# Kernel tuning notes

Hardware: AMD Instinct MI355X
Metric: run time of the kernel (lower is better)

The kernel has to match this reference:

```python
import jax, jax.numpy as jnp
import numpy as np

D_MODEL = 1024
N_HEADS = 16
HEAD_DIM = D_MODEL // N_HEADS


def setup_inputs() -> dict:
    key = jax.random.key(0)
    ks = jax.random.split(key, 10)
    s = 1.0 / np.sqrt(D_MODEL)
    inp = {
        "ts_features": jax.random.normal(ks[0], (8, 512, D_MODEL), dtype=jnp.float32),
        "llm_features": jax.random.normal(ks[1], (8, 2048, D_MODEL), dtype=jnp.float32),
        "q_w": jax.random.uniform(ks[2], (D_MODEL, D_MODEL), jnp.float32, -s, s),
        "q_b": jax.random.uniform(ks[3], (D_MODEL,), jnp.float32, -s, s),
        "k_w": jax.random.uniform(ks[4], (D_MODEL, D_MODEL), jnp.float32, -s, s),
        "k_b": jax.random.uniform(ks[5], (D_MODEL,), jnp.float32, -s, s),
        "v_w": jax.random.uniform(ks[6], (D_MODEL, D_MODEL), jnp.float32, -s, s),
        "v_b": jax.random.uniform(ks[7], (D_MODEL,), jnp.float32, -s, s),
        "o_w": jax.random.uniform(ks[8], (D_MODEL, D_MODEL), jnp.float32, -s, s),
        "o_b": jax.random.uniform(ks[9], (D_MODEL,), jnp.float32, -s, s),
    }
    return inp


def reference(ts_features, llm_features, q_w, q_b, k_w, k_b, v_w, v_b, o_w, o_b):
    B, P, _ = ts_features.shape
    S = llm_features.shape[1]
    # Linear projections (torch Linear: x @ W^T + b); split heads -> [B, H, L, Dh]
    q = (ts_features @ q_w.T + q_b).reshape(B, P, N_HEADS, HEAD_DIM).transpose(0, 2, 1, 3)
    k = (llm_features @ k_w.T + k_b).reshape(B, S, N_HEADS, HEAD_DIM).transpose(0, 2, 1, 3)
    v = (llm_features @ v_w.T + v_b).reshape(B, S, N_HEADS, HEAD_DIM).transpose(0, 2, 1, 3)
    # Full attention: scores [B, H, P, S]
    scores = jnp.einsum("bhpd,bhsd->bhps", q, k) / np.sqrt(HEAD_DIM).astype(np.float32)
    attn = jax.nn.softmax(scores, axis=-1)  # dropout is identity in eval mode
    context = jnp.einsum("bhps,bhsd->bhpd", attn, v)
    context = context.transpose(0, 2, 1, 3).reshape(B, P, D_MODEL)
    return context @ o_w.T + o_b
```

## Files before the change

### kernel.cpp

```cpp
#include <hip/hip_runtime.h>

#define DM 1024
#define B_ 8
#define P_ 512
#define S_ 2048

typedef __bf16 bf16;
typedef __bf16 bf16x4 __attribute__((ext_vector_type(4)));
typedef __bf16 bf16x8 __attribute__((ext_vector_type(8)));
typedef float f32x4 __attribute__((ext_vector_type(4)));
typedef float f32x16 __attribute__((ext_vector_type(16)));

__device__ __forceinline__ void gload_lds16(const void* g, void* l) {
  __builtin_amdgcn_global_load_lds(
      (const __attribute__((address_space(1))) unsigned int*)g,
      (__attribute__((address_space(3))) unsigned int*)l, 16, 0, 0);
}

__device__ __forceinline__ f32x4 mfma16(bf16x8 a, bf16x8 b, f32x4 c) {
  return __builtin_amdgcn_mfma_f32_16x16x32_bf16(a, b, c, 0, 0, 0);
}
__device__ __forceinline__ f32x16 mfma32(bf16x8 a, bf16x8 b, f32x16 c) {
  return __builtin_amdgcn_mfma_f32_32x32x16_bf16(a, b, c, 0, 0, 0);
}

__device__ __forceinline__ unsigned cvt_pk_bf16(float lo, float hi) {
  unsigned r;
  asm("v_cvt_pk_bf16_f32 %0, %1, %2" : "=v"(r) : "v"(lo), "v"(hi));
  return r;
}
__device__ __forceinline__ void plswap(unsigned& a, unsigned& b) {
  asm volatile("s_nop 1\n\tv_permlane32_swap_b32 %0, %1" : "+v"(a), "+v"(b));
}
__device__ __forceinline__ void bar() {
  asm volatile("" ::: "memory");
  __builtin_amdgcn_s_barrier();
  asm volatile("" ::: "memory");
}

union U8 { unsigned u[4]; bf16x8 v; };

#define QSCALE 0.18033688011112042f

__global__ void cvt_all(const float* __restrict__ ts, const float* __restrict__ llm,
                        const float* __restrict__ qw, const float* __restrict__ kw,
                        const float* __restrict__ vw, const float* __restrict__ ow,
                        bf16* __restrict__ ts_o, bf16* __restrict__ llm_o,
                        bf16* __restrict__ qw_o, bf16* __restrict__ kw_o,
                        bf16* __restrict__ vw_o, bf16* __restrict__ ow_o) {
  const int total = 24 << 18;
  int i = blockIdx.x * blockDim.x + threadIdx.x;
  const int stride = gridDim.x * blockDim.x;
  for (; i < total; i += stride) {
    int r = i >> 18;
    const float* in;
    bf16* out;
    int off;
    if (r < 4) { in = ts; out = ts_o; off = i; }
    else if (r < 20) { in = llm; out = llm_o; off = i - (4 << 18); }
    else if (r == 20) { in = qw; out = qw_o; off = i - (20 << 18); }
    else if (r == 21) { in = kw; out = kw_o; off = i - (21 << 18); }
    else if (r == 22) { in = vw; out = vw_o; off = i - (22 << 18); }
    else { in = ow; out = ow_o; off = i - (23 << 18); }
    float4 v = reinterpret_cast<const float4*>(in)[off];
    bf16x4 o;
    o[0] = (bf16)v.x; o[1] = (bf16)v.y; o[2] = (bf16)v.z; o[3] = (bf16)v.w;
    reinterpret_cast<bf16x4*>(out)[off] = o;
  }
}

enum { MODE_F32 = 0, MODE_Q = 1 };

template <int MODE>
__global__ __launch_bounds__(256) void gemm_bt(
    const bf16* __restrict__ A, const bf16* __restrict__ Bw,
    const float* __restrict__ bias, void* __restrict__ out) {
  __shared__ char As[16384];
  __shared__ char Bs[16384];
  const int tid = threadIdx.x;
  const int w = tid >> 6, lane = tid & 63;
  const int g = lane >> 4, l15 = lane & 15;
  const int tn = blockIdx.x, tm = blockIdx.y;
  const int wm = w >> 1, wn = w & 1;

  f32x4 acc[4][4] = {};

  const char* Abase = (const char*)A + (size_t)(tm * 128) * (DM * 2);
  const char* Bbase = (const char*)Bw + (size_t)(tn * 128) * (DM * 2);

  for (int kt = 0; kt < DM / 64; ++kt) {
#pragma unroll
    for (int i = 0; i < 4; ++i) {
      int f = (w * 4 + i) * 1024 + lane * 16;
      int row = f >> 7;
      int kb = f & 127;
      int src = kb ^ ((row & 7) << 4);
      gload_lds16(Abase + (size_t)row * (DM * 2) + kt * 128 + src, As + (w * 4 + i) * 1024);
      gload_lds16(Bbase + (size_t)row * (DM * 2) + kt * 128 + src, Bs + (w * 4 + i) * 1024);
    }
    __syncthreads();
#pragma unroll
    for (int kk = 0; kk < 2; ++kk) {
      bf16x8 af[4], bfr[4];
#pragma unroll
      for (int mi = 0; mi < 4; ++mi) {
        int row = wm * 64 + mi * 16 + l15;
        int off = row * 128 + ((kk * 64 + g * 16) ^ ((row & 7) << 4));
        af[mi] = *reinterpret_cast<const bf16x8*>(As + off);
      }
#pragma unroll
      for (int ni = 0; ni < 4; ++ni) {
        int row = wn * 64 + ni * 16 + l15;
        int off = row * 128 + ((kk * 64 + g * 16) ^ ((row & 7) << 4));
        bfr[ni] = *reinterpret_cast<const bf16x8*>(Bs + off);
      }
#pragma unroll
      for (int mi = 0; mi < 4; ++mi)
#pragma unroll
        for (int ni = 0; ni < 4; ++ni)
          acc[mi][ni] = mfma16(af[mi], bfr[ni], acc[mi][ni]);
    }
    __syncthreads();
  }

#pragma unroll
  for (int mi = 0; mi < 4; ++mi) {
#pragma unroll
    for (int ni = 0; ni < 4; ++ni) {
      const int n = tn * 128 + wn * 64 + ni * 16 + l15;
      const float bn = bias[n];
      const int mb = tm * 128 + wm * 64 + mi * 16 + g * 4;
#pragma unroll
      for (int r = 0; r < 4; ++r) {
        const int m = mb + r;
        const float v = acc[mi][ni][r] + bn;
        if constexpr (MODE == MODE_F32) {
          ((float*)out)[(size_t)m * 1024 + n] = v;
        } else {
          const int b = m >> 9, p = m & 511, h = n >> 6, d = n & 63;
          ((bf16*)out)[((size_t)((b * 16 + h) * 512 + p)) * 64 + d] = (bf16)(v * QSCALE);
        }
      }
    }
  }
}

__global__ __launch_bounds__(512, 2) void gemm256kv(
    const bf16* __restrict__ A, const bf16* __restrict__ Bw,
    const float* __restrict__ kb, const float* __restrict__ vb,
    bf16* __restrict__ Kout, bf16* __restrict__ VTout) {
  __shared__ char lds[131072];
  const int tid = threadIdx.x;
  const int w = tid >> 6, lane = tid & 63;
  const int g = lane >> 4, l15 = lane & 15;
  const int wm = w >> 2, wn = w & 3;

  const int id = blockIdx.x;
  const int nid = (id & 7) * 64 + (id >> 3);
  const int tn = nid & 7, tm = nid >> 3;

  const int f0 = tid * 16, f1 = f0 + 8192;
  const int r0 = f0 >> 7, r1 = f1 >> 7;
  const size_t so0 = (size_t)r0 * 2048 + ((f0 & 127) ^ ((r0 & 7) << 4));
  const size_t so1 = (size_t)r1 * 2048 + ((f1 & 127) ^ ((r1 & 7) << 4));

  const char* Ab = (const char*)A + (size_t)(tm * 256) * 2048;
  const char* Bb = (const char*)Bw + (size_t)(tn * 256) * 2048;

#define STG(OP, HALF, KT)                                                      \
  {                                                                            \
    const char* base = ((OP) ? Bb : Ab) + (size_t)((HALF) * 128) * 2048 +      \
                       (size_t)(KT) * 128;                                     \
    char* dst = lds + (OP) * 65536 + ((((KT) & 1) * 2 + (HALF)) * 16384);      \
    gload_lds16(base + so0, dst + f0);                                         \
    gload_lds16(base + so1, dst + f1);                                         \
  }

  f32x4 acc[8][4] = {};
  bf16x8 a[4][2], b0[2][2], b1[2][2];

#define RD_A(MH)                                                               \
  _Pragma("unroll") for (int mi = 0; mi < 4; ++mi) _Pragma("unroll")           \
      for (int kk = 0; kk < 2; ++kk) {                                         \
    int lr = (MH) * 64 + mi * 16 + l15;                                        \
    int off = (((unsigned)(kt & 1) * 2 + wm) * 16384) + lr * 128 +             \
              ((kk * 64 + g * 16) ^ ((lr & 7) << 4));                          \
    a[mi][kk] = *reinterpret_cast<const bf16x8*>(lds + off);                   \
  }
#define RD_B(NH, DST)                                                          \
  _Pragma("unroll") for (int ni = 0; ni < 2; ++ni) _Pragma("unroll")           \
      for (int kk = 0; kk < 2; ++kk) {                                         \
    int lr = (wn & 1) * 64 + ((NH) * 2 + ni) * 16 + l15;                       \
    int off = 65536 + (((unsigned)(kt & 1) * 2 + (wn >> 1)) * 16384) +         \
              lr * 128 + ((kk * 64 + g * 16) ^ ((lr & 7) << 4));               \
    DST[ni][kk] = *reinterpret_cast<const bf16x8*>(lds + off);                 \
  }
#define MM(MH, NH, B)                                                          \
  __builtin_amdgcn_s_setprio(1);                                              \
  _Pragma("unroll") for (int mi = 0; mi < 4; ++mi) _Pragma("unroll")           \
      for (int ni = 0; ni < 2; ++ni) _Pragma("unroll")                         \
      for (int kk = 0; kk < 2; ++kk)                                           \
          acc[(MH)*4 + mi][(NH)*2 + ni] =                                      \
              mfma16(a[mi][kk], B[ni][kk], acc[(MH)*4 + mi][(NH)*2 + ni]);     \
  __builtin_amdgcn_s_setprio(0);

  STG(0, 0, 0); STG(1, 0, 0); STG(0, 1, 0); STG(1, 1, 0);
  STG(1, 1, 1); STG(0, 0, 1); STG(1, 0, 1);
  asm volatile("s_waitcnt vmcnt(6)" ::: "memory");
  bar();

  for (int kt = 0; kt < 16; ++kt) {
    RD_A(0); RD_B(0, b0);
    if (kt + 1 < 16) STG(0, 1, kt + 1);
    bar();
    MM(0, 0, b0);
    bar();
    RD_B(1, b1);
    bar();
    MM(0, 1, b1);
    bar();
    RD_A(1);
    if (kt + 2 < 16) STG(1, 1, kt + 2);
    bar();
    MM(1, 0, b0);
    bar();
    if (kt + 2 < 16) { STG(0, 0, kt + 2); STG(1, 0, kt + 2); }
    if (kt < 14) {
      asm volatile("s_waitcnt vmcnt(6)" ::: "memory");
    } else {
      asm volatile("s_waitcnt vmcnt(0)" ::: "memory");
    }
    bar();
    MM(1, 1, b1);
    bar();
  }

#pragma unroll
  for (int am = 0; am < 8; ++am) {
#pragma unroll
    for (int an = 0; an < 4; ++an) {
      const int n = tn * 256 + wn * 64 + an * 16 + l15;
      const int mb = tm * 256 + wm * 128 + am * 16 + g * 4;
      const int b = mb >> 11, s = mb & 2047;
      if (n >= 1024) {
        const int h = (n - 1024) >> 6, d = (n - 1024) & 63;
        const float bn = vb[n - 1024];
        bf16x4 pk;
#pragma unroll
        for (int r = 0; r < 4; ++r) pk[r] = (bf16)(acc[am][an][r] + bn);
        *reinterpret_cast<bf16x4*>(VTout + ((size_t)((b * 16 + h) * 64 + d)) * 2048 + s) = pk;
      } else {
        const int h = n >> 6, d = n & 63;
        const float bn = kb[n];
#pragma unroll
        for (int r = 0; r < 4; ++r)
          Kout[((size_t)((b * 16 + h) * 2048 + s + r)) * 64 + d] =
              (bf16)(acc[am][an][r] + bn);
      }
    }
  }
#undef STG
#undef RD_A
#undef RD_B
#undef MM
}

__global__ __launch_bounds__(256) void attn_kernel(
    const bf16* __restrict__ Q, const bf16* __restrict__ K,
    const bf16* __restrict__ VT, bf16* __restrict__ ctx) {
  __shared__ char lds[65536];
  const int tid = threadIdx.x;
  const int w = tid >> 6, lane = tid & 63;
  const int l31 = lane & 31, hi = lane >> 5;

  const int n = blockIdx.x;
  const int xcd = n & 7, mm = n >> 3;
  const int bh = xcd + ((mm >> 2) << 3);
  const int qt = mm & 3;
  const int q0 = qt * 128;

  const char* Kb = (const char*)(K + (size_t)bh * 2048 * 64);
  const char* Vb = (const char*)(VT + (size_t)bh * 64 * 2048);

  const char* Qrow = (const char*)(Q + ((size_t)bh * 512 + q0 + w * 32 + l31) * 64);
  bf16x8 qf[4];
#pragma unroll
  for (int kk = 0; kk < 4; ++kk)
    qf[kk] = *reinterpret_cast<const bf16x8*>(Qrow + kk * 32 + hi * 16);

  float lrun = 0.f;
  f32x16 oacc[2] = {};

#define STAGE(S0, BUF)                                                        \
  {                                                                           \
    _Pragma("unroll") for (int i = 0; i < 4; ++i) {                           \
      int f = i * 4096 + (w * 64 + lane) * 16;                                \
      int krow = f >> 7, kbyte = f & 127;                                     \
      gload_lds16(Kb + (size_t)((S0) + krow) * 128 +                          \
                      (kbyte ^ ((krow & 7) << 4)),                            \
                  (BUF) + i * 4096 + w * 1024);                               \
      int vrow = f >> 8, vbyte = f & 255;                                     \
      gload_lds16(Vb + (size_t)vrow * 4096 + (size_t)(S0) * 2 +               \
                      (vbyte ^ ((vrow & 7) << 4)),                            \
                  (BUF) + 16384 + i * 4096 + w * 1024);                       \
    }                                                                         \
  }

#define SUBTILE(T2, CUR)                                                      \
  {                                                                           \
    f32x16 sa[2] = {};                                                        \
    __builtin_amdgcn_s_setprio(1);                                            \
    _Pragma("unroll") for (int t = 0; t < 2; ++t) {                           \
      _Pragma("unroll") for (int kk = 0; kk < 4; ++kk) {                      \
        int row = (T2) * 64 + t * 32 + l31;                                   \
        int off = row * 128 + ((kk * 32 + hi * 16) ^ ((row & 7) << 4));       \
        bf16x8 kf = *reinterpret_cast<const bf16x8*>((CUR) + off);            \
        sa[t] = mfma32(kf, qf[kk], sa[t]);                                    \
      }                                                                       \
    }                                                                         \
    __builtin_amdgcn_s_setprio(0);                                            \
    bf16x8 vf[8];                                                             \
    _Pragma("unroll") for (int dt = 0; dt < 2; ++dt)                          \
        _Pragma("unroll") for (int ks = 0; ks < 4; ++ks) {                    \
      int row = dt * 32 + l31;                                                \
      int col = (T2) * 128 + ks * 32 + hi * 16;                               \
      int off = 16384 + row * 256 + (col ^ ((row & 7) << 4));                 \
      vf[dt * 4 + ks] = *reinterpret_cast<const bf16x8*>((CUR) + off);        \
    }                                                                         \
    bf16x8 pf[4];                                                             \
    _Pragma("unroll") for (int t = 0; t < 2; ++t)                             \
        _Pragma("unroll") for (int h2 = 0; h2 < 2; ++h2) {                    \
      float p[8];                                                             \
      _Pragma("unroll") for (int j = 0; j < 8; ++j) {                         \
        p[j] = __builtin_amdgcn_exp2f(sa[t][8 * h2 + j]);                     \
        lrun += p[j];                                                         \
      }                                                                       \
      unsigned a0 = cvt_pk_bf16(p[0], p[1]);                                  \
      unsigned a1 = cvt_pk_bf16(p[2], p[3]);                                  \
      unsigned a2 = cvt_pk_bf16(p[4], p[5]);                                  \
      unsigned a3 = cvt_pk_bf16(p[6], p[7]);                                  \
      plswap(a0, a2);                                                         \
      plswap(a1, a3);                                                         \
      U8 u;                                                                   \
      u.u[0] = a0; u.u[1] = a1; u.u[2] = a2; u.u[3] = a3;                     \
      pf[t * 2 + h2] = u.v;                                                   \
    }                                                                         \
    __builtin_amdgcn_s_setprio(1);                                            \
    _Pragma("unroll") for (int dt = 0; dt < 2; ++dt)                          \
        _Pragma("unroll") for (int ks = 0; ks < 4; ++ks)                      \
            oacc[dt] = mfma32(vf[dt * 4 + ks], pf[ks], oacc[dt]);             \
    __builtin_amdgcn_s_setprio(0);                                            \
  }

  STAGE(0, lds);

  for (int c = 0; c < 16; ++c) {
    char* cur = lds + (c & 1) * 32768;
    if (c + 1 < 16) {
      STAGE((c + 1) * 128, lds + ((c + 1) & 1) * 32768);
      asm volatile("s_waitcnt vmcnt(8)" ::: "memory");
    } else {
      asm volatile("s_waitcnt vmcnt(0)" ::: "memory");
    }
    bar();

    SUBTILE(0, cur);
    SUBTILE(1, cur);

    bar();
  }

  lrun += __shfl_xor(lrun, 32);
  const float inv = 1.0f / lrun;
  const int b = bh >> 4, h = bh & 15;
  const int prow = q0 + w * 32 + l31;
  bf16* dst = ctx + ((size_t)(b * 512 + prow)) * 1024 + h * 64;
#pragma unroll
  for (int dt = 0; dt < 2; ++dt)
#pragma unroll
    for (int g4 = 0; g4 < 4; ++g4) {
      bf16x4 pk4;
#pragma unroll
      for (int r = 0; r < 4; ++r) pk4[r] = (bf16)(oacc[dt][g4 * 4 + r] * inv);
      *reinterpret_cast<bf16x4*>(dst + dt * 32 + g4 * 8 + hi * 4) = pk4;
    }
#undef STAGE
#undef SUBTILE
}

extern "C" void kernel_launch(void* const* d_in, const int* in_sizes, int n_in,
                              void* d_out, int out_size, void* d_ws, size_t ws_size,
                              hipStream_t stream) {
  const float* ts = (const float*)d_in[0];
  const float* llm = (const float*)d_in[1];
  const float* qw = (const float*)d_in[2];
  const float* qb = (const float*)d_in[3];
  const float* kw = (const float*)d_in[4];
  const float* kb = (const float*)d_in[5];
  const float* vw = (const float*)d_in[6];
  const float* vb = (const float*)d_in[7];
  const float* ow = (const float*)d_in[8];
  const float* ob = (const float*)d_in[9];

  char* ws = (char*)d_ws;
  bf16* ts_bf = (bf16*)(ws + (0ull << 20));
  bf16* llm_bf = (bf16*)(ws + (8ull << 20));
  bf16* qw_bf = (bf16*)(ws + (40ull << 20));
  bf16* kw_bf = (bf16*)(ws + (42ull << 20));
  bf16* vw_bf = (bf16*)(ws + (44ull << 20));
  bf16* ow_bf = (bf16*)(ws + (46ull << 20));
  bf16* Qb = (bf16*)(ws + (48ull << 20));
  bf16* Kb = (bf16*)(ws + (56ull << 20));
  bf16* VTb = (bf16*)(ws + (88ull << 20));
  bf16* ctx = (bf16*)(ws + (120ull << 20));

  cvt_all<<<2048, 256, 0, stream>>>(ts, llm, qw, kw, vw, ow,
                                    ts_bf, llm_bf, qw_bf, kw_bf, vw_bf, ow_bf);

  gemm_bt<MODE_Q><<<dim3(8, 32), 256, 0, stream>>>(ts_bf, qw_bf, qb, Qb);
  gemm256kv<<<512, 512, 0, stream>>>(llm_bf, kw_bf, kb, vb, Kb, VTb);
  attn_kernel<<<512, 256, 0, stream>>>(Qb, Kb, VTb, ctx);
  gemm_bt<MODE_F32><<<dim3(8, 32), 256, 0, stream>>>(ctx, ow_bf, ob, (void*)d_out);
}
```

Measured before the change: 193.7 us.

## Split attention over key halves and double query rows per wave with combine pass

The attention kernel now has each wave process 64 query rows (two 32-row groups) that share each K/V fragment load. The key sequence is split into two halves across blocks, so the grid stays at 512 blocks. Each block writes unnormalized fp32 partial outputs and row sums, and a new combine kernel adds the halves, normalizes, and writes bf16 context. This halves LDS K/V traffic per query row, at the cost of an extra kernel launch, fp32 partial round-trip traffic, and higher register pressure with launch bounds of 2. The partial buffers reuse workspace from the ts/llm bf16 copies, which are already consumed by then.

```diff
diff --git a/kernel.cpp b/kernel.cpp
--- a/kernel.cpp
+++ b/kernel.cpp
@@ -265,31 +265,36 @@
 #undef MM
 }
 
-__global__ __launch_bounds__(256) void attn_kernel(
+__global__ __launch_bounds__(256, 2) void attn_kernel(
     const bf16* __restrict__ Q, const bf16* __restrict__ K,
-    const bf16* __restrict__ VT, bf16* __restrict__ ctx) {
+    const bf16* __restrict__ VT, float* __restrict__ Opart,
+    float* __restrict__ lpart) {
   __shared__ char lds[65536];
   const int tid = threadIdx.x;
   const int w = tid >> 6, lane = tid & 63;
   const int l31 = lane & 31, hi = lane >> 5;
 
   const int n = blockIdx.x;
-  const int xcd = n & 7, mm = n >> 3;
-  const int bh = xcd + ((mm >> 2) << 3);
-  const int qt = mm & 3;
-  const int q0 = qt * 128;
+  const int wid = (n & 7) * 64 + (n >> 3);
+  const int bh = wid >> 2;
+  const int qh = (wid >> 1) & 1;
+  const int sh = wid & 1;
+  const int q0 = qh * 256;
+  const int sbase = sh * 1024;
 
   const char* Kb = (const char*)(K + (size_t)bh * 2048 * 64);
   const char* Vb = (const char*)(VT + (size_t)bh * 64 * 2048);
 
-  const char* Qrow = (const char*)(Q + ((size_t)bh * 512 + q0 + w * 32 + l31) * 64);
-  bf16x8 qf[4];
-#pragma unroll
-  for (int kk = 0; kk < 4; ++kk)
-    qf[kk] = *reinterpret_cast<const bf16x8*>(Qrow + kk * 32 + hi * 16);
-
-  float lrun = 0.f;
-  f32x16 oacc[2] = {};
+  const char* QrowA = (const char*)(Q + ((size_t)bh * 512 + q0 + w * 64 + l31) * 64);
+  bf16x8 qfA[4], qfB[4];
+#pragma unroll
+  for (int kk = 0; kk < 4; ++kk) {
+    qfA[kk] = *reinterpret_cast<const bf16x8*>(QrowA + kk * 32 + hi * 16);
+    qfB[kk] = *reinterpret_cast<const bf16x8*>(QrowA + 4096 + kk * 32 + hi * 16);
+  }
+
+  float lrunA = 0.f, lrunB = 0.f;
+  f32x16 oaccA[2] = {}, oaccB[2] = {};
 
 #define STAGE(S0, BUF)                                                        \
   {                                                                           \
@@ -306,58 +311,69 @@
     }                                                                         \
   }
 
+#define SOFTMAX(SA, PF, LRUN)                                                 \
+  _Pragma("unroll") for (int t = 0; t < 2; ++t)                               \
+      _Pragma("unroll") for (int h2 = 0; h2 < 2; ++h2) {                      \
+    float p[8];                                                               \
+    _Pragma("unroll") for (int j = 0; j < 8; ++j) {                           \
+      p[j] = __builtin_amdgcn_exp2f(SA[t][8 * h2 + j]);                       \
+      LRUN += p[j];                                                           \
+    }                                                                         \
+    unsigned a0 = cvt_pk_bf16(p[0], p[1]);                                    \
+    unsigned a1 = cvt_pk_bf16(p[2], p[3]);                                    \
+    unsigned a2 = cvt_pk_bf16(p[4], p[5]);                                    \
+    unsigned a3 = cvt_pk_bf16(p[6], p[7]);                                    \
+    plswap(a0, a2);                                                           \
+    plswap(a1, a3);                                                           \
+    U8 u;                                                                     \
+    u.u[0] = a0; u.u[1] = a1; u.u[2] = a2; u.u[3] = a3;                       \
+    PF[t * 2 + h2] = u.v;                                                     \
+  }
+
 #define SUBTILE(T2, CUR)                                                      \
   {                                                                           \
+    bf16x8 kf[8];                                                             \
+    _Pragma("unroll") for (int t = 0; t < 2; ++t)                             \
+        _Pragma("unroll") for (int kk = 0; kk < 4; ++kk) {                    \
+      int row = (T2) * 64 + t * 32 + l31;                                     \
+      int off = row * 128 + ((kk * 32 + hi * 16) ^ ((row & 7) << 4));         \
+      kf[t * 4 + kk] = *reinterpret_cast<const bf16x8*>((CUR) + off);         \
+    }                                                                         \
     f32x16 sa[2] = {};                                                        \
     __builtin_amdgcn_s_setprio(1);                                            \
-    _Pragma("unroll") for (int t = 0; t < 2; ++t) {                           \
-      _Pragma("unroll") for (int kk = 0; kk < 4; ++kk) {                      \
-        int row = (T2) * 64 + t * 32 + l31;                                   \
-        int off = row * 128 + ((kk * 32 + hi * 16) ^ ((row & 7) << 4));       \
-        bf16x8 kf = *reinterpret_cast<const bf16x8*>((CUR) + off);            \
-        sa[t] = mfma32(kf, qf[kk], sa[t]);                                    \
-      }                                                                       \
-    }                                                                         \
+    _Pragma("unroll") for (int t = 0; t < 2; ++t)                             \
+        _Pragma("unroll") for (int kk = 0; kk < 4; ++kk)                      \
+            sa[t] = mfma32(kf[t * 4 + kk], qfA[kk], sa[t]);                   \
     __builtin_amdgcn_s_setprio(0);                                            \
-    bf16x8 vf[8];                                                             \
+    bf16x8 pfA[4];                                                            \
+    SOFTMAX(sa, pfA, lrunA);                                                  \
+    f32x16 sb[2] = {};                                                        \
+    __builtin_amdgcn_s_setprio(1);                                            \
+    _Pragma("unroll") for (int t = 0; t < 2; ++t)                             \
+        _Pragma("unroll") for (int kk = 0; kk < 4; ++kk)                      \
+            sb[t] = mfma32(kf[t * 4 + kk], qfB[kk], sb[t]);                   \
+    __builtin_amdgcn_s_setprio(0);                                            \
+    bf16x8 pfB[4];                                                            \
+    SOFTMAX(sb, pfB, lrunB);                                                  \
+    __builtin_amdgcn_s_setprio(1);                                            \
     _Pragma("unroll") for (int dt = 0; dt < 2; ++dt)                          \
         _Pragma("unroll") for (int ks = 0; ks < 4; ++ks) {                    \
       int row = dt * 32 + l31;                                                \
       int col = (T2) * 128 + ks * 32 + hi * 16;                               \
       int off = 16384 + row * 256 + (col ^ ((row & 7) << 4));                 \
-      vf[dt * 4 + ks] = *reinterpret_cast<const bf16x8*>((CUR) + off);        \
+      bf16x8 vf = *reinterpret_cast<const bf16x8*>((CUR) + off);              \
+      oaccA[dt] = mfma32(vf, pfA[ks], oaccA[dt]);                             \
+      oaccB[dt] = mfma32(vf, pfB[ks], oaccB[dt]);                             \
     }                                                                         \
-    bf16x8 pf[4];                                                             \
-    _Pragma("unroll") for (int t = 0; t < 2; ++t)                             \
-        _Pragma("unroll") for (int h2 = 0; h2 < 2; ++h2) {                    \
-      float p[8];                                                             \
-      _Pragma("unroll") for (int j = 0; j < 8; ++j) {                         \
-        p[j] = __builtin_amdgcn_exp2f(sa[t][8 * h2 + j]);                     \
-        lrun += p[j];                                                         \
-      }                                                                       \
-      unsigned a0 = cvt_pk_bf16(p[0], p[1]);                                  \
-      unsigned a1 = cvt_pk_bf16(p[2], p[3]);                                  \
-      unsigned a2 = cvt_pk_bf16(p[4], p[5]);                                  \
-      unsigned a3 = cvt_pk_bf16(p[6], p[7]);                                  \
-      plswap(a0, a2);                                                         \
-      plswap(a1, a3);                                                         \
-      U8 u;                                                                   \
-      u.u[0] = a0; u.u[1] = a1; u.u[2] = a2; u.u[3] = a3;                     \
-      pf[t * 2 + h2] = u.v;                                                   \
-    }                                                                         \
-    __builtin_amdgcn_s_setprio(1);                                            \
-    _Pragma("unroll") for (int dt = 0; dt < 2; ++dt)                          \
-        _Pragma("unroll") for (int ks = 0; ks < 4; ++ks)                      \
-            oacc[dt] = mfma32(vf[dt * 4 + ks], pf[ks], oacc[dt]);             \
     __builtin_amdgcn_s_setprio(0);                                            \
   }
 
-  STAGE(0, lds);
-
-  for (int c = 0; c < 16; ++c) {
+  STAGE(sbase, lds);
+
+  for (int c = 0; c < 8; ++c) {
     char* cur = lds + (c & 1) * 32768;
-    if (c + 1 < 16) {
-      STAGE((c + 1) * 128, lds + ((c + 1) & 1) * 32768);
+    if (c + 1 < 8) {
+      STAGE(sbase + (c + 1) * 128, lds + ((c + 1) & 1) * 32768);
       asm volatile("s_waitcnt vmcnt(8)" ::: "memory");
     } else {
       asm volatile("s_waitcnt vmcnt(0)" ::: "memory");
@@ -370,22 +386,59 @@
     bar();
   }
 
-  lrun += __shfl_xor(lrun, 32);
-  const float inv = 1.0f / lrun;
-  const int b = bh >> 4, h = bh & 15;
-  const int prow = q0 + w * 32 + l31;
-  bf16* dst = ctx + ((size_t)(b * 512 + prow)) * 1024 + h * 64;
+  lrunA += __shfl_xor(lrunA, 32);
+  lrunB += __shfl_xor(lrunB, 32);
+  const size_t rowgA = (size_t)bh * 512 + q0 + w * 64 + l31;
+  const size_t rowgB = rowgA + 32;
+  float* OdA = Opart + ((size_t)sh * 65536 + rowgA) * 64;
+  float* OdB = Opart + ((size_t)sh * 65536 + rowgB) * 64;
+  if (hi == 0) {
+    lpart[(size_t)sh * 65536 + rowgA] = lrunA;
+    lpart[(size_t)sh * 65536 + rowgB] = lrunB;
+  }
 #pragma unroll
   for (int dt = 0; dt < 2; ++dt)
 #pragma unroll
     for (int g4 = 0; g4 < 4; ++g4) {
-      bf16x4 pk4;
-#pragma unroll
-      for (int r = 0; r < 4; ++r) pk4[r] = (bf16)(oacc[dt][g4 * 4 + r] * inv);
-      *reinterpret_cast<bf16x4*>(dst + dt * 32 + g4 * 8 + hi * 4) = pk4;
+      f32x4 stA, stB;
+#pragma unroll
+      for (int r = 0; r < 4; ++r) {
+        stA[r] = oaccA[dt][g4 * 4 + r];
+        stB[r] = oaccB[dt][g4 * 4 + r];
+      }
+      *reinterpret_cast<f32x4*>(OdA + dt * 32 + g4 * 8 + hi * 4) = stA;
+      *reinterpret_cast<f32x4*>(OdB + dt * 32 + g4 * 8 + hi * 4) = stB;
     }
 #undef STAGE
+#undef SOFTMAX
 #undef SUBTILE
+}
+
+__global__ __launch_bounds__(256) void combine_kernel(
+    const float* __restrict__ Opart, const float* __restrict__ lpart,
+    bf16* __restrict__ ctx) {
+  int idx = blockIdx.x * blockDim.x + threadIdx.x;
+  int row = idx >> 3, dc = (idx & 7) * 8;
+  const float* o0 = Opart + (size_t)row * 64 + dc;
+  const float* o1 = o0 + (size_t)65536 * 64;
+  float inv = 1.0f / (lpart[row] + lpart[65536 + row]);
+  float4 a0 = *(const float4*)o0;
+  float4 a1 = *(const float4*)(o0 + 4);
+  float4 c0 = *(const float4*)o1;
+  float4 c1 = *(const float4*)(o1 + 4);
+  int bh = row >> 9, p = row & 511;
+  int b = bh >> 4, h = bh & 15;
+  bf16* dst = ctx + ((size_t)(b * 512 + p)) * 1024 + h * 64 + dc;
+  bf16x8 o;
+  o[0] = (bf16)((a0.x + c0.x) * inv);
+  o[1] = (bf16)((a0.y + c0.y) * inv);
+  o[2] = (bf16)((a0.z + c0.z) * inv);
+  o[3] = (bf16)((a0.w + c0.w) * inv);
+  o[4] = (bf16)((a1.x + c1.x) * inv);
+  o[5] = (bf16)((a1.y + c1.y) * inv);
+  o[6] = (bf16)((a1.z + c1.z) * inv);
+  o[7] = (bf16)((a1.w + c1.w) * inv);
+  *reinterpret_cast<bf16x8*>(dst) = o;
 }
 
 extern "C" void kernel_launch(void* const* d_in, const int* in_sizes, int n_in,
@@ -413,12 +466,15 @@
   bf16* Kb = (bf16*)(ws + (56ull << 20));
   bf16* VTb = (bf16*)(ws + (88ull << 20));
   bf16* ctx = (bf16*)(ws + (120ull << 20));
+  float* Opart = (float*)(ws + (0ull << 20));
+  float* lpart = (float*)(ws + (32ull << 20));
 
   cvt_all<<<2048, 256, 0, stream>>>(ts, llm, qw, kw, vw, ow,
                                     ts_bf, llm_bf, qw_bf, kw_bf, vw_bf, ow_bf);
 
   gemm_bt<MODE_Q><<<dim3(8, 32), 256, 0, stream>>>(ts_bf, qw_bf, qb, Qb);
   gemm256kv<<<512, 512, 0, stream>>>(llm_bf, kw_bf, kb, vb, Kb, VTb);
-  attn_kernel<<<512, 256, 0, stream>>>(Qb, Kb, VTb, ctx);
+  attn_kernel<<<512, 256, 0, stream>>>(Qb, Kb, VTb, Opart, lpart);
+  combine_kernel<<<2048, 256, 0, stream>>>(Opart, lpart, ctx);
   gemm_bt<MODE_F32><<<dim3(8, 32), 256, 0, stream>>>(ctx, ow_bf, ob, (void*)d_out);
 }
```

Measured after the change: 230.6 us. 19.1% more time.
